# Performance work log

Measured on AMD Instinct MI355X. Metric: run time of the kernel, lower is better.

## Reference

```python
import jax, jax.numpy as jnp
import numpy as np

VOCAB, X, H, C_CLS = 32000, 300, 512, 5
B, N_LEAVES = 256, 256  # complete binary trees, depth 9, 511 nodes/tree

def setup_inputs() -> dict:
    key = jax.random.key(0)
    ks = jax.random.split(key, 10)
    s = lambda k, shp, fan: jax.random.normal(k, shp, jnp.float32) * (1.0 / np.sqrt(fan))
    return {
        'wordid': jax.random.randint(ks[0], (B, N_LEAVES), 0, VOCAB),
        'emb': jax.random.normal(ks[1], (VOCAB, X), jnp.float32) * 0.1,
        'W_iou_w': s(ks[2], (3 * H, X), X),
        'W_iou_b': jnp.zeros((3 * H,), jnp.float32),
        'U_iou_w': s(ks[3], (3 * H, 2 * H), 2 * H),
        'U_iou_b': jnp.zeros((3 * H,), jnp.float32),
        'U_f_w': s(ks[4], (2 * H, 2 * H), 2 * H),
        'U_f_b': jnp.zeros((2 * H,), jnp.float32),
        'lin_w': s(ks[5], (C_CLS, H), H),
        'lin_b': jnp.zeros((C_CLS,), jnp.float32),
    }

def _cell(iou, c_f):
    i, o, u = jnp.split(iou, 3, axis=-1)
    c = jax.nn.sigmoid(i) * jnp.tanh(u) + c_f
    h = jax.nn.sigmoid(o) * jnp.tanh(c)
    return h, c

def reference(wordid, emb, W_iou_w, W_iou_b, U_iou_w, U_iou_b, U_f_w, U_f_b, lin_w, lin_b):
    b, n = wordid.shape
    # leaves: is_leaf=1 -> iou = W_iou(x), c_f = 0
    x = emb[wordid]                                   # [B, L, X]
    iou = x @ W_iou_w.T + W_iou_b                     # [B, L, 3H]
    h, c = _cell(iou, 0.0)
    hs = [h]
    # internal levels: reduce over exactly 2 children (binary TreeLSTM)
    while h.shape[1] > 1:
        m = h.shape[1] // 2
        h_cat = h.reshape(b, m, 2 * H)                # concat of 2 children
        c_pair = c.reshape(b, m, 2, H)
        f = jax.nn.sigmoid(h_cat @ U_f_w.T + U_f_b).reshape(b, m, 2, H)
        c_f = jnp.sum(f * c_pair, axis=2)             # [B, m, H]
        iou = h_cat @ U_iou_w.T + U_iou_b             # is_leaf=0 branch
        h, c = _cell(iou, c_f)
        hs.append(h)
    h_all = jnp.concatenate(hs, axis=1)               # [B, 2L-1, H], leaves-first topo order
    # dropout is identity at inference
    logits = h_all @ lin_w.T + lin_b                  # [B, 2L-1, num_classes]
    return logits
```

## Files before the change

### kernel.cpp

```cpp
#include <hip/hip_runtime.h>
#include <hip/hip_bf16.h>


typedef __bf16 bf16;
typedef bf16  bf16x8 __attribute__((ext_vector_type(8)));
typedef float f32x4  __attribute__((ext_vector_type(4)));

__device__ __forceinline__ float sigm(float x){ return 1.0f/(1.0f + __expf(-x)); }
__device__ __forceinline__ float tanh_f(float x){ return 1.0f - 2.0f/(__expf(2.0f*x)+1.0f); }

__device__ __forceinline__ void gload16(const bf16* g, bf16* l){
  __builtin_amdgcn_global_load_lds(
      (const __attribute__((address_space(1))) void*)g,
      (__attribute__((address_space(3))) void*)l, 16, 0, 0);
}

#define FENCE_VM(N) do{ asm volatile("s_waitcnt vmcnt(" #N ")" ::: "memory"); \
  __builtin_amdgcn_sched_barrier(0); __builtin_amdgcn_s_barrier(); \
  __builtin_amdgcn_sched_barrier(0); }while(0)
#define FENCE_LGKM do{ asm volatile("s_waitcnt lgkmcnt(0)" ::: "memory"); \
  __builtin_amdgcn_sched_barrier(0); __builtin_amdgcn_s_barrier(); \
  __builtin_amdgcn_sched_barrier(0); }while(0)

__global__ void cvt_all(const float* __restrict__ Wiou, const float* __restrict__ Uiou,
                        const float* __restrict__ Uf, const float* __restrict__ emb,
                        bf16* __restrict__ Wpad, bf16* __restrict__ Uall,
                        bf16* __restrict__ embp){
  const int b = blockIdx.x, t = threadIdx.x;
  if (b < 1536){
    Wpad[b*320 + t] = (bf16)(t < 300 ? Wiou[b*300 + t] : 0.f);
  } else if (b < 1536 + 32000){
    const int r = b - 1536;
    embp[(size_t)r*320 + t] = (bf16)(t < 300 ? emb[(size_t)r*300 + t] : 0.f);
  } else {
    const size_t i = (size_t)(b - 33536)*320 + t;
    if (i < (size_t)1536*1024) Uall[i] = (bf16)Uiou[i];
    else                       Uall[i] = (bf16)Uf[i - (size_t)1536*1024];
  }
}

__global__ __launch_bounds__(256, 2)
void leaf128_kernel(const int* __restrict__ wordid, const bf16* __restrict__ embp,
                    const bf16* __restrict__ Wpad, const float* __restrict__ Wb,
                    bf16* __restrict__ hcur, float* __restrict__ ccur)
{
  __shared__ bf16 lsA[2][128*32];
  __shared__ bf16 lsB[2][192*32];
  const int t = threadIdx.x;
  const int mrow0 = blockIdx.x*128, nblk = blockIdx.y*64;
  const int lane16 = t&15, quad = (t&63)>>4, w = t>>6;

  const int lrow = t>>2;
  const int qsw  = ((t&3) ^ ((t>>3)&3))*8;
  const int wb   = (t & 192)*8;

  const int wid0 = wordid[mrow0 + lrow];
  const int wid1 = wordid[mrow0 + 64 + lrow];
  const bf16* srcA0 = embp + (size_t)wid0*320 + qsw;
  const bf16* srcA1 = embp + (size_t)wid1*320 + qsw;
  const bf16* srcB0 = Wpad + (size_t)(0*512 + nblk + lrow)*320 + qsw;
  const bf16* srcB1 = Wpad + (size_t)(1*512 + nblk + lrow)*320 + qsw;
  const bf16* srcB2 = Wpad + (size_t)(2*512 + nblk + lrow)*320 + qsw;

  const int sA   = (t>>1)&3;
  const int aoff = lane16*32 + ((quad ^ sA)*8);
  const int boff = (w*16 + lane16)*32 + ((quad ^ sA)*8);

  f32x4 acc[3][8];
  const f32x4 zero = {0.f,0.f,0.f,0.f};
  #pragma unroll
  for(int o=0;o<3;o++){
    #pragma unroll
    for(int rt=0;rt<8;rt++) acc[o][rt]=zero;
  }

  {
    gload16(srcA0     , lsA[0] + wb);        gload16(srcA1     , lsA[0] + 2048 + wb);
    gload16(srcB0     , lsB[0] + wb);        gload16(srcB1     , lsB[0] + 2048 + wb);
    gload16(srcB2     , lsB[0] + 4096 + wb);
    gload16(srcA0 + 32, lsA[1] + wb);        gload16(srcA1 + 32, lsA[1] + 2048 + wb);
    gload16(srcB0 + 32, lsB[1] + wb);        gload16(srcB1 + 32, lsB[1] + 2048 + wb);
    gload16(srcB2 + 32, lsB[1] + 4096 + wb);
  }
  FENCE_VM(5);

  for (int ks = 0; ks < 10; ks++){
    const int cur = ks & 1;
    bf16x8 bfrag[3], afrag[8];
    #pragma unroll
    for(int g=0;g<3;g++) bfrag[g] = *(const bf16x8*)&lsB[cur][g*2048 + boff];
    #pragma unroll
    for(int rt=0;rt<8;rt++) afrag[rt] = *(const bf16x8*)&lsA[cur][rt*512 + aoff];
    FENCE_LGKM;
    if (ks < 8){
      const int k0 = (ks+2)*32;
      gload16(srcA0 + k0, lsA[cur] + wb);        gload16(srcA1 + k0, lsA[cur] + 2048 + wb);
      gload16(srcB0 + k0, lsB[cur] + wb);        gload16(srcB1 + k0, lsB[cur] + 2048 + wb);
      gload16(srcB2 + k0, lsB[cur] + 4096 + wb);
    }
    __builtin_amdgcn_s_setprio(1);
    #pragma unroll
    for(int rt=0;rt<8;rt++){
      #pragma unroll
      for(int g=0;g<3;g++)
        acc[g][rt] = __builtin_amdgcn_mfma_f32_16x16x32_bf16(afrag[rt], bfrag[g], acc[g][rt], 0,0,0);
    }
    __builtin_amdgcn_s_setprio(0);
    if (ks < 8)      FENCE_VM(5);
    else if (ks < 9) FENCE_VM(0);
  }
  const int j = nblk + w*16 + lane16;
  const float bi=Wb[j], bo=Wb[512+j], bu=Wb[1024+j];
  #pragma unroll
  for(int rt=0;rt<8;rt++){
    #pragma unroll
    for(int reg=0;reg<4;reg++){
      const int row = mrow0 + rt*16 + quad*4 + reg;
      float iv=acc[0][rt][reg]+bi, ov=acc[1][rt][reg]+bo, uv=acc[2][rt][reg]+bu;
      float c = sigm(iv)*tanh_f(uv);
      float h = sigm(ov)*tanh_f(c);
      ccur[(size_t)row*512 + j] = c;
      hcur[(size_t)row*512 + j] = (bf16)h;
    }
  }
}

__global__ __launch_bounds__(256, 3)
void level_kernel(const bf16* __restrict__ hprev, bf16* __restrict__ hcur,
                  const float* __restrict__ cprev, float* __restrict__ ccur,
                  const bf16* __restrict__ Uall, const float* __restrict__ Uioub,
                  const float* __restrict__ Ufb)
{
  __shared__ bf16 lsA[2][64*32];
  __shared__ bf16 lsB[2][320*32];
  const int t = threadIdx.x;
  const int mrow0 = blockIdx.x*64, nblk = blockIdx.y*64;
  const int lane16 = t&15, quad = (t&63)>>4, w = t>>6;

  const int lrow = t>>2;
  const int qsw  = ((t&3) ^ ((t>>3)&3))*8;
  const int wb   = (t & 192)*8;

  const bf16* srcA0 = hprev + (size_t)(mrow0 + lrow)*1024 + qsw;
  const bf16* srcB0 = Uall + (size_t)(0*512 + nblk + lrow)*1024 + qsw;
  const bf16* srcB1 = Uall + (size_t)(1*512 + nblk + lrow)*1024 + qsw;
  const bf16* srcB2 = Uall + (size_t)(2*512 + nblk + lrow)*1024 + qsw;
  const bf16* srcB3 = Uall + (size_t)(3*512 + nblk + lrow)*1024 + qsw;
  const bf16* srcB4 = Uall + (size_t)(4*512 + nblk + lrow)*1024 + qsw;

  const int sA   = (t>>1)&3;
  const int aoff = lane16*32 + ((quad ^ sA)*8);
  const int boff = (w*16 + lane16)*32 + ((quad ^ sA)*8);

#define LV64_DMA(buf, k0) do{ \
  gload16(srcA0 + (k0), lsA[buf] + wb); \
  gload16(srcB0 + (k0), lsB[buf] + wb);        gload16(srcB1 + (k0), lsB[buf] + 2048 + wb); \
  gload16(srcB2 + (k0), lsB[buf] + 4096 + wb); gload16(srcB3 + (k0), lsB[buf] + 6144 + wb); \
  gload16(srcB4 + (k0), lsB[buf] + 8192 + wb); }while(0)

  f32x4 acc[5][4];
  const f32x4 zero = {0.f,0.f,0.f,0.f};
  #pragma unroll
  for(int o=0;o<5;o++){
    #pragma unroll
    for(int rt=0;rt<4;rt++) acc[o][rt]=zero;
  }

  LV64_DMA(0, 0); LV64_DMA(1, 32);
  FENCE_VM(6);

  for (int ks = 0; ks < 32; ks++){
    const int cur = ks & 1;
    bf16x8 bfrag[5], afrag[4];
    #pragma unroll
    for(int g=0;g<5;g++) bfrag[g] = *(const bf16x8*)&lsB[cur][g*2048 + boff];
    #pragma unroll
    for(int rt=0;rt<4;rt++) afrag[rt] = *(const bf16x8*)&lsA[cur][rt*512 + aoff];
    FENCE_LGKM;
    if (ks < 30){
      LV64_DMA(cur, (ks+2)*32);
    }
    __builtin_amdgcn_s_setprio(1);
    #pragma unroll
    for(int rt=0;rt<4;rt++){
      #pragma unroll
      for(int g=0;g<5;g++)
        acc[g][rt] = __builtin_amdgcn_mfma_f32_16x16x32_bf16(afrag[rt], bfrag[g], acc[g][rt], 0,0,0);
    }
    __builtin_amdgcn_s_setprio(0);
    if (ks < 30)       FENCE_VM(6);
    else if (ks < 31)  FENCE_VM(0);
  }

  const int j = nblk + w*16 + lane16;
  const float bi =Uioub[j], bo=Uioub[512+j], bu=Uioub[1024+j];
  const float bfl=Ufb[j],   bfr=Ufb[512+j];
  #pragma unroll
  for(int rt=0;rt<4;rt++){
    #pragma unroll
    for(int reg=0;reg<4;reg++){
      const int row = mrow0 + rt*16 + quad*4 + reg;
      float iv=acc[0][rt][reg]+bi, ov=acc[1][rt][reg]+bo, uv=acc[2][rt][reg]+bu;
      float fl=acc[3][rt][reg]+bfl, fr=acc[4][rt][reg]+bfr;
      float cl = cprev[((size_t)row*2  )*512 + j];
      float cr = cprev[((size_t)row*2+1)*512 + j];
      float cf = sigm(fl)*cl + sigm(fr)*cr;
      float c  = sigm(iv)*tanh_f(uv) + cf;
      float h  = sigm(ov)*tanh_f(c);
      ccur[(size_t)row*512 + j] = c;
      hcur[(size_t)row*512 + j] = (bf16)h;
    }
  }
#undef LV64_DMA
}

__global__ __launch_bounds__(256, 2)
void level128_kernel(const bf16* __restrict__ hprev, bf16* __restrict__ hcur,
                     const float* __restrict__ cprev, float* __restrict__ ccur,
                     const bf16* __restrict__ Uall, const float* __restrict__ Uioub,
                     const float* __restrict__ Ufb)
{
  __shared__ bf16 lsA[2][128*32];
  __shared__ bf16 lsB[2][320*32];
  const int t = threadIdx.x;
  const int mrow0 = blockIdx.x*128, nblk = blockIdx.y*64;
  const int lane16 = t&15, quad = (t&63)>>4, w = t>>6;

  const int lrow = t>>2;
  const int qsw  = ((t&3) ^ ((t>>3)&3))*8;
  const int wb   = (t & 192)*8;

  const bf16* srcA0 = hprev + (size_t)(mrow0 + lrow)*1024 + qsw;
  const bf16* srcA1 = hprev + (size_t)(mrow0 + 64 + lrow)*1024 + qsw;
  const bf16* srcB0 = Uall + (size_t)(0*512 + nblk + lrow)*1024 + qsw;
  const bf16* srcB1 = Uall + (size_t)(1*512 + nblk + lrow)*1024 + qsw;
  const bf16* srcB2 = Uall + (size_t)(2*512 + nblk + lrow)*1024 + qsw;
  const bf16* srcB3 = Uall + (size_t)(3*512 + nblk + lrow)*1024 + qsw;
  const bf16* srcB4 = Uall + (size_t)(4*512 + nblk + lrow)*1024 + qsw;

  const int sA   = (t>>1)&3;
  const int aoff = lane16*32 + ((quad ^ sA)*8);
  const int boff = (w*16 + lane16)*32 + ((quad ^ sA)*8);

#define LVL_DMA(buf, k0) do{ \
  gload16(srcA0 + (k0), lsA[buf] + wb);        gload16(srcA1 + (k0), lsA[buf] + 2048 + wb); \
  gload16(srcB0 + (k0), lsB[buf] + wb);        gload16(srcB1 + (k0), lsB[buf] + 2048 + wb); \
  gload16(srcB2 + (k0), lsB[buf] + 4096 + wb); gload16(srcB3 + (k0), lsB[buf] + 6144 + wb); \
  gload16(srcB4 + (k0), lsB[buf] + 8192 + wb); }while(0)

  f32x4 acc[5][8];
  const f32x4 zero = {0.f,0.f,0.f,0.f};
  #pragma unroll
  for(int o=0;o<5;o++){
    #pragma unroll
    for(int rt=0;rt<8;rt++) acc[o][rt]=zero;
  }

  LVL_DMA(0, 0); LVL_DMA(1, 32);
  FENCE_VM(7);

  for (int ks = 0; ks < 32; ks++){
    const int cur = ks & 1;
    bf16x8 bfrag[5], afrag[8];
    #pragma unroll
    for(int g=0;g<5;g++) bfrag[g] = *(const bf16x8*)&lsB[cur][g*2048 + boff];
    #pragma unroll
    for(int rt=0;rt<8;rt++) afrag[rt] = *(const bf16x8*)&lsA[cur][rt*512 + aoff];
    FENCE_LGKM;
    if (ks < 30){
      LVL_DMA(cur, (ks+2)*32);
    }
    __builtin_amdgcn_s_setprio(1);
    #pragma unroll
    for(int rt=0;rt<8;rt++){
      #pragma unroll
      for(int g=0;g<5;g++)
        acc[g][rt] = __builtin_amdgcn_mfma_f32_16x16x32_bf16(afrag[rt], bfrag[g], acc[g][rt], 0,0,0);
    }
    __builtin_amdgcn_s_setprio(0);
    if (ks < 30)       FENCE_VM(7);
    else if (ks < 31)  FENCE_VM(0);
  }

  const int j = nblk + w*16 + lane16;
  const float bi =Uioub[j], bo=Uioub[512+j], bu=Uioub[1024+j];
  const float bfl=Ufb[j],   bfr=Ufb[512+j];
  #pragma unroll
  for(int rt=0;rt<8;rt++){
    #pragma unroll
    for(int reg=0;reg<4;reg++){
      const int row = mrow0 + rt*16 + quad*4 + reg;
      float iv=acc[0][rt][reg]+bi, ov=acc[1][rt][reg]+bo, uv=acc[2][rt][reg]+bu;
      float fl=acc[3][rt][reg]+bfl, fr=acc[4][rt][reg]+bfr;
      float cl = cprev[((size_t)row*2  )*512 + j];
      float cr = cprev[((size_t)row*2+1)*512 + j];
      float cf = sigm(fl)*cl + sigm(fr)*cr;
      float c  = sigm(iv)*tanh_f(uv) + cf;
      float h  = sigm(ov)*tanh_f(c);
      ccur[(size_t)row*512 + j] = c;
      hcur[(size_t)row*512 + j] = (bf16)h;
    }
  }
#undef LVL_DMA
}

__global__ __launch_bounds__(256)
void logits_kernel(const bf16* __restrict__ h, const float* __restrict__ linw,
                   const float* __restrict__ linb, float* __restrict__ out,
                   int rowbase, int lgm, int mask, int off){
  const int row = blockIdx.x*4 + (threadIdx.x>>6);
  const int l = threadIdx.x & 63;
  bf16x8 hv = *(const bf16x8*)(h + (size_t)row*512 + l*8);
  float hf[8];
  #pragma unroll
  for(int jj=0;jj<8;jj++) hf[jj] = (float)hv[jj];
  float s[5];
  #pragma unroll
  for(int c=0;c<5;c++){
    const f32x4 w0 = *(const f32x4*)(linw + c*512 + l*8);
    const f32x4 w1 = *(const f32x4*)(linw + c*512 + l*8 + 4);
    float a = 0.f;
    #pragma unroll
    for(int jj=0;jj<4;jj++) a += hf[jj]*w0[jj] + hf[4+jj]*w1[jj];
    s[c]=a;
  }
  #pragma unroll
  for(int o=32;o>0;o>>=1){
    #pragma unroll
    for(int c=0;c<5;c++) s[c] += __shfl_down(s[c], o, 64);
  }
  if (l==0){
    const int g = rowbase + row;
    const int node = (g>>lgm)*511 + off + (g&mask);
    #pragma unroll
    for(int c=0;c<5;c++) out[(size_t)node*5+c] = s[c] + linb[c];
  }
}

__global__ __launch_bounds__(256)
void logits2_kernel(const bf16* __restrict__ ha, int rows_a, int lgm_a, int mask_a, int off_a,
                    const bf16* __restrict__ hb, int lgm_b, int mask_b, int off_b,
                    const float* __restrict__ linw, const float* __restrict__ linb,
                    float* __restrict__ out){
  const int row = blockIdx.x*4 + (threadIdx.x>>6);
  const int l = threadIdx.x & 63;
  const bf16* hrow; int g, lgm, mask, off;
  if (row < rows_a){ hrow = ha + (size_t)row*512;            g = row;           lgm=lgm_a; mask=mask_a; off=off_a; }
  else             { hrow = hb + (size_t)(row-rows_a)*512;   g = row - rows_a;  lgm=lgm_b; mask=mask_b; off=off_b; }
  bf16x8 hv = *(const bf16x8*)(hrow + l*8);
  float hf[8];
  #pragma unroll
  for(int jj=0;jj<8;jj++) hf[jj] = (float)hv[jj];
  float s[5];
  #pragma unroll
  for(int c=0;c<5;c++){
    const f32x4 w0 = *(const f32x4*)(linw + c*512 + l*8);
    const f32x4 w1 = *(const f32x4*)(linw + c*512 + l*8 + 4);
    float a = 0.f;
    #pragma unroll
    for(int jj=0;jj<4;jj++) a += hf[jj]*w0[jj] + hf[4+jj]*w1[jj];
    s[c]=a;
  }
  #pragma unroll
  for(int o=32;o>0;o>>=1){
    #pragma unroll
    for(int c=0;c<5;c++) s[c] += __shfl_down(s[c], o, 64);
  }
  if (l==0){
    const int node = (g>>lgm)*511 + off + (g&mask);
    #pragma unroll
    for(int c=0;c<5;c++) out[(size_t)node*5+c] = s[c] + linb[c];
  }
}

__global__ void zero_out(float* out, int n){
  int i = blockIdx.x*256 + threadIdx.x;
  if (i < n) out[i] = 0.f;
}

extern "C" void kernel_launch(void* const* d_in, const int* in_sizes, int n_in,
                              void* d_out, int out_size, void* d_ws, size_t ws_size,
                              hipStream_t stream)
{
  const int*   wordid = (const int*)d_in[0];
  const float* emb    = (const float*)d_in[1];
  const float* Wiou   = (const float*)d_in[2];
  const float* Wioub  = (const float*)d_in[3];
  const float* Uiou   = (const float*)d_in[4];
  const float* Uioub  = (const float*)d_in[5];
  const float* Uf     = (const float*)d_in[6];
  const float* Ufb    = (const float*)d_in[7];
  const float* linw   = (const float*)d_in[8];
  const float* linb   = (const float*)d_in[9];
  float* out = (float*)d_out;

  const size_t oWPD  = 0;
  const size_t oUALL = oWPD  + (size_t)1536*320*2;
  const size_t oEMB  = oUALL + (size_t)2560*1024*2;
  const size_t oH1   = oEMB  + (size_t)32000*320*2;
  const size_t oC1   = oH1   + (size_t)32768*512*2;
  const size_t oH0   = oC1   + (size_t)32768*512*4;
  size_t R0 = 0;
  {
    const size_t t2 = oH0 + (size_t)32768*512*(2+4);
    const size_t t4 = oH0 + (size_t)16384*512*(2+4);
    const size_t t8 = oH0 + (size_t) 8192*512*(2+4);
    if      (ws_size >= t2) R0 = 32768;
    else if (ws_size >= t4) R0 = 16384;
    else if (ws_size >= t8) R0 = 8192;
  }
  if (R0 == 0){
    zero_out<<<(out_size+255)/256, 256, 0, stream>>>(out, out_size);
    return;
  }

  char* ws = (char*)d_ws;
  bf16*  Wpad = (bf16*)(ws + oWPD);
  bf16*  Uall = (bf16*)(ws + oUALL);
  bf16*  embp = (bf16*)(ws + oEMB);
  bf16*  h1   = (bf16*)(ws + oH1);
  float* c1   = (float*)(ws + oC1);
  bf16*  h0   = (bf16*)(ws + oH0);
  float* c0   = (float*)(ws + oH0 + R0*1024);

  cvt_all<<<41728, 320, 0, stream>>>(Wiou, Uiou, Uf, emb, Wpad, Uall, embp);

  const int offs[9] = {0,256,384,448,480,496,504,508,510};
  const int nchunk = (int)(65536 / R0);

  for (int ch = 0; ch < nchunk; ch++){
    const int* wid = wordid + (size_t)ch*R0;
    leaf128_kernel<<<dim3((int)(R0/128), 8), 256, 0, stream>>>(wid, embp, Wpad, Wioub,
                                                               h0, c0);
    logits_kernel<<<(int)(R0/4), 256, 0, stream>>>(h0, linw, linb, out,
                                                   (int)(ch*R0), 8, 255, 0);
    bf16*  h1c = h1 + (size_t)ch*(R0/2)*512;
    float* c1c = c1 + (size_t)ch*(R0/2)*512;
    const int orows = (int)(R0/2);
    level128_kernel<<<dim3(orows/128, 8), 256, 0, stream>>>(h0, h1c, c0, c1c,
                                                            Uall, Uioub, Ufb);
  }

  for (int lv = 2; lv <= 8; lv++){
    const int rows = 65536 >> lv;
    const bf16*  hin  = (lv & 1) ? h0 : h1;
    bf16*        hout = (lv & 1) ? h1 : h0;
    const float* cin  = (lv & 1) ? c0 : c1;
    float*       cout = (lv & 1) ? c1 : c0;
    if (rows >= 8192)
      level128_kernel<<<dim3(rows/128, 8), 256, 0, stream>>>(hin, hout, cin, cout,
                                                             Uall, Uioub, Ufb);
    else
      level_kernel<<<dim3(rows/64, 8), 256, 0, stream>>>(hin, hout, cin, cout,
                                                         Uall, Uioub, Ufb);
    if ((lv & 1) == 0){
      const int rows_a = 65536 >> (lv-1);
      const int rows_b = rows;
      logits2_kernel<<<(rows_a + rows_b)/4, 256, 0, stream>>>(
          h1, rows_a, 8-(lv-1), (256>>(lv-1))-1, offs[lv-1],
          h0,         8-lv,     (256>>lv)-1,     offs[lv],
          linw, linb, out);
    }
  }
}
```

Measured before the change: 795.1 us.

## Process both LDS buffers per barrier stage in leaf and level GEMM loops

Restructures the double-buffered K loops in the leaf and level kernels. Each stage now waits for both buffers, reads fragments from both into registers, reissues DMA for the next two K slices, then runs twice as many MFMAs. This halves the number of barrier and waitcnt sync points per K loop. In exchange it roughly doubles live fragment registers, which could hurt occupancy under launch_bounds(256,3). It also removes overlap between the loads and the wait at the top of each stage, since every stage waits for all outstanding loads.

Measured after the change: 1.349 ms. 1.7x slower.

```diff
diff --git a/kernel.cpp b/kernel.cpp
--- a/kernel.cpp
+++ b/kernel.cpp
@@ -66,6 +66,11 @@
   const int aoff = lane16*32 + ((quad ^ sA)*8);
   const int boff = (w*16 + lane16)*32 + ((quad ^ sA)*8);
 
+#define LEAF_DMA(buf, k0) do{ \
+  gload16(srcA0 + (k0), lsA[buf] + wb);        gload16(srcA1 + (k0), lsA[buf] + 2048 + wb); \
+  gload16(srcB0 + (k0), lsB[buf] + wb);        gload16(srcB1 + (k0), lsB[buf] + 2048 + wb); \
+  gload16(srcB2 + (k0), lsB[buf] + 4096 + wb); }while(0)
+
   f32x4 acc[3][8];
   const f32x4 zero = {0.f,0.f,0.f,0.f};
   #pragma unroll
@@ -74,40 +79,37 @@
     for(int rt=0;rt<8;rt++) acc[o][rt]=zero;
   }
 
-  {
-    gload16(srcA0     , lsA[0] + wb);        gload16(srcA1     , lsA[0] + 2048 + wb);
-    gload16(srcB0     , lsB[0] + wb);        gload16(srcB1     , lsB[0] + 2048 + wb);
-    gload16(srcB2     , lsB[0] + 4096 + wb);
-    gload16(srcA0 + 32, lsA[1] + wb);        gload16(srcA1 + 32, lsA[1] + 2048 + wb);
-    gload16(srcB0 + 32, lsB[1] + wb);        gload16(srcB1 + 32, lsB[1] + 2048 + wb);
-    gload16(srcB2 + 32, lsB[1] + 4096 + wb);
-  }
-  FENCE_VM(5);
-
-  for (int ks = 0; ks < 10; ks++){
-    const int cur = ks & 1;
-    bf16x8 bfrag[3], afrag[8];
-    #pragma unroll
-    for(int g=0;g<3;g++) bfrag[g] = *(const bf16x8*)&lsB[cur][g*2048 + boff];
-    #pragma unroll
-    for(int rt=0;rt<8;rt++) afrag[rt] = *(const bf16x8*)&lsA[cur][rt*512 + aoff];
-    FENCE_LGKM;
-    if (ks < 8){
-      const int k0 = (ks+2)*32;
-      gload16(srcA0 + k0, lsA[cur] + wb);        gload16(srcA1 + k0, lsA[cur] + 2048 + wb);
-      gload16(srcB0 + k0, lsB[cur] + wb);        gload16(srcB1 + k0, lsB[cur] + 2048 + wb);
-      gload16(srcB2 + k0, lsB[cur] + 4096 + wb);
+  LEAF_DMA(0, 0); LEAF_DMA(1, 32);
+
+  for (int ss = 0; ss < 5; ss++){
+    FENCE_VM(0);
+    bf16x8 fB[3], fA[8], gB[3], gA[8];
+    #pragma unroll
+    for(int g=0;g<3;g++) fB[g] = *(const bf16x8*)&lsB[0][g*2048 + boff];
+    #pragma unroll
+    for(int rt=0;rt<8;rt++) fA[rt] = *(const bf16x8*)&lsA[0][rt*512 + aoff];
+    #pragma unroll
+    for(int g=0;g<3;g++) gB[g] = *(const bf16x8*)&lsB[1][g*2048 + boff];
+    #pragma unroll
+    for(int rt=0;rt<8;rt++) gA[rt] = *(const bf16x8*)&lsA[1][rt*512 + aoff];
+    if (ss < 4){
+      FENCE_LGKM;
+      LEAF_DMA(0, ss*64 + 64); LEAF_DMA(1, ss*64 + 96);
     }
     __builtin_amdgcn_s_setprio(1);
     #pragma unroll
     for(int rt=0;rt<8;rt++){
       #pragma unroll
       for(int g=0;g<3;g++)
-        acc[g][rt] = __builtin_amdgcn_mfma_f32_16x16x32_bf16(afrag[rt], bfrag[g], acc[g][rt], 0,0,0);
+        acc[g][rt] = __builtin_amdgcn_mfma_f32_16x16x32_bf16(fA[rt], fB[g], acc[g][rt], 0,0,0);
+    }
+    #pragma unroll
+    for(int rt=0;rt<8;rt++){
+      #pragma unroll
+      for(int g=0;g<3;g++)
+        acc[g][rt] = __builtin_amdgcn_mfma_f32_16x16x32_bf16(gA[rt], gB[g], acc[g][rt], 0,0,0);
     }
     __builtin_amdgcn_s_setprio(0);
-    if (ks < 8)      FENCE_VM(5);
-    else if (ks < 9) FENCE_VM(0);
   }
   const int j = nblk + w*16 + lane16;
   const float bi=Wb[j], bo=Wb[512+j], bu=Wb[1024+j];
@@ -123,6 +125,7 @@
       hcur[(size_t)row*512 + j] = (bf16)h;
     }
   }
+#undef LEAF_DMA
 }
 
 __global__ __launch_bounds__(256, 3)
@@ -257,29 +260,36 @@
   }
 
   LVL_DMA(0, 0); LVL_DMA(1, 32);
-  FENCE_VM(7);
-
-  for (int ks = 0; ks < 32; ks++){
-    const int cur = ks & 1;
-    bf16x8 bfrag[5], afrag[8];
-    #pragma unroll
-    for(int g=0;g<5;g++) bfrag[g] = *(const bf16x8*)&lsB[cur][g*2048 + boff];
-    #pragma unroll
-    for(int rt=0;rt<8;rt++) afrag[rt] = *(const bf16x8*)&lsA[cur][rt*512 + aoff];
-    FENCE_LGKM;
-    if (ks < 30){
-      LVL_DMA(cur, (ks+2)*32);
+
+  for (int ss = 0; ss < 16; ss++){
+    FENCE_VM(0);
+    bf16x8 fB[5], fA[8], gB[5], gA[8];
+    #pragma unroll
+    for(int g=0;g<5;g++) fB[g] = *(const bf16x8*)&lsB[0][g*2048 + boff];
+    #pragma unroll
+    for(int rt=0;rt<8;rt++) fA[rt] = *(const bf16x8*)&lsA[0][rt*512 + aoff];
+    #pragma unroll
+    for(int g=0;g<5;g++) gB[g] = *(const bf16x8*)&lsB[1][g*2048 + boff];
+    #pragma unroll
+    for(int rt=0;rt<8;rt++) gA[rt] = *(const bf16x8*)&lsA[1][rt*512 + aoff];
+    if (ss < 15){
+      FENCE_LGKM;
+      LVL_DMA(0, ss*64 + 64); LVL_DMA(1, ss*64 + 96);
     }
     __builtin_amdgcn_s_setprio(1);
     #pragma unroll
     for(int rt=0;rt<8;rt++){
       #pragma unroll
       for(int g=0;g<5;g++)
-        acc[g][rt] = __builtin_amdgcn_mfma_f32_16x16x32_bf16(afrag[rt], bfrag[g], acc[g][rt], 0,0,0);
+        acc[g][rt] = __builtin_amdgcn_mfma_f32_16x16x32_bf16(fA[rt], fB[g], acc[g][rt], 0,0,0);
+    }
+    #pragma unroll
+    for(int rt=0;rt<8;rt++){
+      #pragma unroll
+      for(int g=0;g<5;g++)
+        acc[g][rt] = __builtin_amdgcn_mfma_f32_16x16x32_bf16(gA[rt], gB[g], acc[g][rt], 0,0,0);
     }
     __builtin_amdgcn_s_setprio(0);
-    if (ks < 30)       FENCE_VM(7);
-    else if (ks < 31)  FENCE_VM(0);
   }
 
   const int j = nblk + w*16 + lane16;
```
